# Kernel tuning notes

Measured on AMD Instinct MI355X. Metric: run time of the kernel, lower is better.

The kernel has to match this reference:

```python
import jax, jax.numpy as jnp
import numpy as np

K = 256      # embedding size k
STATE = 128  # latent state size
IN = 64      # external input size
OBS = 64     # observation size
L = 512      # sequence length (time-major)
B = 256      # batch size


def _glorot(key, shape):
    return jax.random.normal(key, shape, dtype=jnp.float32) / float(np.sqrt(shape[0]))


def setup_inputs():
    key = jax.random.key(0)
    ks = jax.random.split(key, 12)
    p = {}
    p["external_input_seq"] = jax.random.normal(ks[0], (L, B, IN), dtype=jnp.float32)
    p["observations_seq"] = jax.random.normal(ks[1], (L, B, OBS), dtype=jnp.float32)
    p["eps"] = jax.random.normal(ks[2], (L, B, STATE), dtype=jnp.float32)  # reparam noise
    # PreProcess: Linear + tanh
    p["Wu"] = _glorot(ks[3], (IN, K)); p["bu"] = jnp.zeros((K,), jnp.float32)
    p["Wx"] = _glorot(ks[4], (OBS, K)); p["bx"] = jnp.zeros((K,), jnp.float32)
    # input_rnn: vanilla tanh RNN, 1 layer, k -> k
    p["W_ih"] = _glorot(ks[5], (K, K)); p["b_ih"] = jnp.zeros((K,), jnp.float32)
    p["W_hh"] = _glorot(ks[6], (K, K)); p["b_hh"] = jnp.zeros((K,), jnp.float32)
    # posterior_a_layer: MLP(2k, k, k, 1) = Linear -> tanh -> Linear
    p["Wa1"] = _glorot(ks[7], (2 * K, K)); p["ba1"] = jnp.zeros((K,), jnp.float32)
    p["Wa2"] = _glorot(ks[8], (K, K)); p["ba2"] = jnp.zeros((K,), jnp.float32)

    def dblock_params(k1, in_dim, hid, out):
        kk = jax.random.split(k1, 4)
        return (_glorot(kk[0], (in_dim, hid)), jnp.zeros((hid,), jnp.float32),
                _glorot(kk[1], (in_dim, hid)), jnp.zeros((hid,), jnp.float32),
                _glorot(kk[2], (hid, out)), jnp.zeros((out,), jnp.float32),
                _glorot(kk[3], (hid, out)), jnp.zeros((out,), jnp.float32))

    names = ["f1_W", "f1_b", "f2_W", "f2_b", "mu_W", "mu_b", "ls_W", "ls_b"]
    for pref, kk in (("post_", ks[9]), ("prior_", ks[10])):
        vals = dblock_params(kk, STATE + K, 2 * K, STATE)
        for n, v in zip(names, vals):
            p[pref + n] = v
    return p


def _dblock(x, f1_W, f1_b, f2_W, f2_b, mu_W, mu_b, ls_W, ls_b):
    # TD-VAE DBlock: gated hidden, then mu / logsigma heads
    t = jnp.tanh(x @ f1_W + f1_b) * jax.nn.sigmoid(x @ f2_W + f2_b)
    return t @ mu_W + mu_b, t @ ls_W + ls_b


def reference(external_input_seq, observations_seq, eps, Wu, bu, Wx, bx,
              W_ih, b_ih, W_hh, b_hh, Wa1, ba1, Wa2, ba2,
              post_f1_W, post_f1_b, post_f2_W, post_f2_b, post_mu_W, post_mu_b, post_ls_W, post_ls_b,
              prior_f1_W, prior_f1_b, prior_f2_W, prior_f2_b, prior_mu_W, prior_mu_b, prior_ls_W, prior_ls_b):
    batch = external_input_seq.shape[1]
    u_emb = jnp.tanh(external_input_seq @ Wu + bu)   # [L,B,K]
    x_emb = jnp.tanh(observations_seq @ Wx + bx)     # [L,B,K]

    # input_rnn (tanh RNN) over time, d0 = 0 (memory_state=None)
    def rnn_step(d, x):
        d_new = jnp.tanh(x @ W_ih + b_ih + d @ W_hh + b_hh)
        return d_new, d_new
    d0 = jnp.zeros((batch, W_hh.shape[0]), dtype=u_emb.dtype)
    dn, d_seq = jax.lax.scan(rnn_step, d0, u_emb)    # dn [B,K], d_seq [L,B,K]

    # posterior_a_layer: pointwise MLP; flip(0) then flip(0) is a no-op for a pointwise map
    ad = jnp.concatenate([d_seq, x_emb], axis=-1)    # [L,B,2K]
    a_seq = jnp.tanh(ad @ Wa1 + ba1) @ Wa2 + ba2     # [L,B,K]

    state_size = post_mu_W.shape[1]
    z0 = jnp.zeros((batch, state_size), dtype=u_emb.dtype)

    def step(z_prev, inp):
        a_t, d_t, e_t = inp
        mean_res, logsigma = _dblock(jnp.concatenate([z_prev, a_t], axis=-1),
                                     post_f1_W, post_f1_b, post_f2_W, post_f2_b,
                                     post_mu_W, post_mu_b, post_ls_W, post_ls_b)
        prior_mean = _dblock(jnp.concatenate([z_prev, d_t], axis=-1),
                             prior_f1_W, prior_f1_b, prior_f2_W, prior_f2_b,
                             prior_mu_W, prior_mu_b, prior_ls_W, prior_ls_b)[0]
        mu = prior_mean + mean_res
        # cov = diag(exp(logsigma)) -> std = exp(0.5*logsigma); reparameterized sample
        z_new = mu + jnp.exp(0.5 * logsigma) * e_t
        return z_new, (mu, logsigma)

    zn, (state_mu, state_logsigma) = jax.lax.scan(step, z0, (a_seq, d_seq, eps))
    return state_mu, state_logsigma, dn, zn
```

## Files before the change

kernel.cpp:

```cpp
#include <hip/hip_runtime.h>

#define LSEQ 512
#define BATCH 256
#define KDIM 256
#define STATE 128

using f32x4  = __attribute__((ext_vector_type(4))) float;
using short8 = __attribute__((ext_vector_type(8))) short;
using u32x2  = __attribute__((ext_vector_type(2))) unsigned int;
using u32x4  = __attribute__((ext_vector_type(4))) unsigned int;

__device__ __forceinline__ float bf2f(unsigned short u){
  return __uint_as_float(((unsigned int)u) << 16);
}
__device__ __forceinline__ unsigned short f2bf(float f){
  unsigned int u = __float_as_uint(f);
  u += 0x7FFFu + ((u >> 16) & 1u);
  return (unsigned short)(u >> 16);
}
__device__ __forceinline__ float fast_tanh(float x){
  float ax = fabsf(x);
  float e  = __expf(2.0f * ax);
  float t  = 1.0f - 2.0f / (e + 1.0f);
  return copysignf(t, x);
}
__device__ __forceinline__ float fast_sig(float x){
  return 1.0f / (1.0f + __expf(-x));
}
__device__ __forceinline__ f32x4 mfma16(short8 a, short8 b, f32x4 c){
  return __builtin_amdgcn_mfma_f32_16x16x32_bf16(a, b, c, 0, 0, 0);
}

__device__ __forceinline__ int swz128 (int b){ return b ^ ((((b >> 7) & 7) << 4)); }
__device__ __forceinline__ int swz256 (int b){ return b ^ ((((b >> 8) & 7) << 4)); }
__device__ __forceinline__ int swz512 (int b){ return b ^ ((((b >> 9) & 7) << 4)); }

__device__ __forceinline__ void st_b128_ic(void* p, u32x4 v){
  asm volatile("global_store_dwordx4 %0, %1, off sc0 sc1" :: "v"(p), "v"(v) : "memory");
}
__device__ __forceinline__ void st_b64_ic(void* p, u32x2 v){
  asm volatile("global_store_dwordx2 %0, %1, off sc0 sc1" :: "v"(p), "v"(v) : "memory");
}
#define LD2_IC(dst, p) asm volatile("global_load_dwordx2 %0, %1, off sc0 sc1" : "=v"(dst) : "v"(p) : "memory")

__device__ __forceinline__ f32x4 cvt4(u32x2 q){
  f32x4 r;
  r[0] = __uint_as_float(q[0] << 16);
  r[1] = __uint_as_float(q[0] & 0xFFFF0000u);
  r[2] = __uint_as_float(q[1] << 16);
  r[3] = __uint_as_float(q[1] & 0xFFFF0000u);
  return r;
}

struct WDesc { const float* src; unsigned short* dst; int K, N, ld, rowoff, coloff; };
struct WDescs { WDesc d[24]; };

__global__ __launch_bounds__(256,4) void convert_weights(WDescs ds){
  WDesc w = ds.d[blockIdx.y];
  int total = w.K * w.N;
  int idx = blockIdx.x * 256 + threadIdx.x;
  if (idx < total){
    int n = idx / w.K;
    int k = idx - n * w.K;
    w.dst[idx] = f2bf(w.src[(size_t)(w.rowoff + k) * w.ld + w.coloff + n]);
  }
}

__global__ __launch_bounds__(256,1) void init_flags(int* flags){
  flags[blockIdx.x * 256 + threadIdx.x] = 0;
}

__global__ __launch_bounds__(256,4) void compose_GA(
    const float* __restrict__ Wa2, const float* __restrict__ ba2,
    const unsigned short* __restrict__ fAp,
    const float* __restrict__ pf1b, const float* __restrict__ pf2b,
    unsigned short* __restrict__ GA, float* __restrict__ gb)
{
  const int n = blockIdx.x;
  const int k2 = threadIdx.x;
  const unsigned short* fr = fAp + (size_t)n * 256;
  const float* wr = Wa2 + (size_t)k2 * 256;
  float s = 0.f;
  for (int j = 0; j < 256; j++) s += wr[j] * bf2f(fr[j]);
  GA[(size_t)n * 256 + k2] = f2bf(s);
  if (k2 == 0){
    float b = 0.f;
    for (int j = 0; j < 256; j++) b += ba2[j] * bf2f(fr[j]);
    gb[n] = b + ((n < 512) ? pf1b[n] : pf2b[n - 512]);
  }
}

struct GArg {
  const void* A; const unsigned short* Bt; const float* bias; const float* bias2;
  unsigned short* C; int lda, ldc, coff, K, act, a_f32;
};
struct GArg2 {
  const unsigned short* A; const unsigned short* Bt; const float* bias; const float* bias2;
  unsigned short* C; int lda, ldc, coff, K, act;
};

__device__ void gemm_multi_body(const GArg ga, int bx, int by, int tid, char* lsraw){
  char* lsA = lsraw;
  char* lsB = lsraw + 16384;
  const int wave = tid >> 6, lane = tid & 63;
  const int col_l = lane & 15, rgrp = lane >> 4;
  const int m0 = bx * 128, n0 = by * 128;
  const int wm = (wave >> 1) * 64, wn = (wave & 1) * 64;

  f32x4 acc[4][4];
  const f32x4 z4 = {0.f,0.f,0.f,0.f};
  #pragma unroll
  for (int i=0;i<4;i++){ acc[i][0]=z4; acc[i][1]=z4; acc[i][2]=z4; acc[i][3]=z4; }

  const int srow = tid >> 1;
  const int sbe  = (tid & 1) * 32;

  for (int k0 = 0; k0 < ga.K; k0 += 64){
    uint4 av[4], bv[4];
    if (ga.a_f32){
      const float* Ap = (const float*)ga.A + (size_t)(m0 + srow) * ga.lda + k0 + sbe;
      uint4 fv[8];
      #pragma unroll
      for (int i=0;i<8;i++) fv[i] = *(const uint4*)((const char*)Ap + i*16);
      #pragma unroll
      for (int i=0;i<4;i++){
        const float* f = (const float*)&fv[i*2];
        uint4 o;
        o.x = (unsigned)f2bf(f[0]) | ((unsigned)f2bf(f[1]) << 16);
        o.y = (unsigned)f2bf(f[2]) | ((unsigned)f2bf(f[3]) << 16);
        o.z = (unsigned)f2bf(f[4]) | ((unsigned)f2bf(f[5]) << 16);
        o.w = (unsigned)f2bf(f[6]) | ((unsigned)f2bf(f[7]) << 16);
        av[i] = o;
      }
    } else {
      const unsigned short* Ap = (const unsigned short*)ga.A + (size_t)(m0 + srow) * ga.lda + k0 + sbe;
      #pragma unroll
      for (int i=0;i<4;i++) av[i] = *(const uint4*)((const char*)Ap + i*16);
    }
    const unsigned short* Bp = ga.Bt + (size_t)(n0 + srow) * ga.K + k0 + sbe;
    #pragma unroll
    for (int i=0;i<4;i++) bv[i] = *(const uint4*)((const char*)Bp + i*16);

    __syncthreads();
    #pragma unroll
    for (int i=0;i<4;i++){
      *(uint4*)(lsA + swz128(srow*128 + sbe*2 + i*16)) = av[i];
      *(uint4*)(lsB + swz128(srow*128 + sbe*2 + i*16)) = bv[i];
    }
    __syncthreads();
    #pragma unroll
    for (int kk=0; kk<2; kk++){
      short8 af[4], bfr[4];
      #pragma unroll
      for (int mt=0; mt<4; mt++)
        af[mt] = *(const short8*)(lsA + swz128((wm + mt*16 + col_l)*128 + kk*64 + rgrp*16));
      #pragma unroll
      for (int nt=0; nt<4; nt++)
        bfr[nt] = *(const short8*)(lsB + swz128((wn + nt*16 + col_l)*128 + kk*64 + rgrp*16));
      #pragma unroll
      for (int mt=0; mt<4; mt++)
        #pragma unroll
        for (int nt=0; nt<4; nt++)
          acc[mt][nt] = mfma16(af[mt], bfr[nt], acc[mt][nt]);
    }
  }
  #pragma unroll
  for (int nt=0; nt<4; nt++){
    int col = n0 + wn + nt*16 + col_l;
    const float* bsrc = (col < 512) ? ga.bias : ga.bias2;
    float bb = bsrc ? bsrc[col & 511] : 0.0f;
    #pragma unroll
    for (int mt=0; mt<4; mt++){
      #pragma unroll
      for (int r=0; r<4; r++){
        int row = m0 + wm + mt*16 + rgrp*4 + r;
        float v = acc[mt][nt][r] + bb;
        if (ga.act == 1) v = fast_tanh(v);
        ga.C[(size_t)row * ga.ldc + ga.coff + col] = f2bf(v);
      }
    }
  }
}

__device__ void gemm_glds_body(const GArg2 ga, int bx, int by, int tid, char* lsraw){
  const int wave = tid >> 6, lane = tid & 63;
  const int col_l = lane & 15, rgrp = lane >> 4;
  const int m0 = bx * 128, n0 = by * 128;
  const int wm = (wave >> 1) * 64, wn = (wave & 1) * 64;

  const int lrow = lane >> 3;
  const int scol = (((lane & 7) ^ lrow) << 3);

  auto STAGE = [&](int k0, int buf){
    #pragma unroll
    for (int c = 0; c < 4; c++){
      int srow = wave*32 + c*8 + lrow;
      const unsigned short* pa = ga.A  + (size_t)(m0 + srow) * ga.lda + k0 + scol;
      const unsigned short* pb = ga.Bt + (size_t)(n0 + srow) * ga.K  + k0 + scol;
      __builtin_amdgcn_global_load_lds(
          (const __attribute__((address_space(1))) unsigned int*)pa,
          (__attribute__((address_space(3))) unsigned int*)(lsraw + buf*32768 + wave*4096 + c*1024),
          16, 0, 0);
      __builtin_amdgcn_global_load_lds(
          (const __attribute__((address_space(1))) unsigned int*)pb,
          (__attribute__((address_space(3))) unsigned int*)(lsraw + buf*32768 + 16384 + wave*4096 + c*1024),
          16, 0, 0);
    }
  };

  f32x4 acc[4][4];
  const f32x4 z4 = {0.f,0.f,0.f,0.f};
  #pragma unroll
  for (int i=0;i<4;i++){ acc[i][0]=z4; acc[i][1]=z4; acc[i][2]=z4; acc[i][3]=z4; }

  const int niter = ga.K >> 6;
  STAGE(0, 0);

  for (int i = 0; i < niter; i++){
    if (i + 1 < niter){
      STAGE((i+1)*64, (i+1) & 1);
      asm volatile("s_waitcnt vmcnt(8)" ::: "memory");
    } else {
      asm volatile("s_waitcnt vmcnt(0)" ::: "memory");
    }
    __syncthreads();
    const char* la = lsraw + (i&1)*32768;
    const char* lb = la + 16384;
    #pragma unroll
    for (int kk=0; kk<2; kk++){
      short8 af[4], bfr[4];
      #pragma unroll
      for (int mt=0; mt<4; mt++)
        af[mt] = *(const short8*)(la + swz128((wm + mt*16 + col_l)*128 + kk*64 + rgrp*16));
      #pragma unroll
      for (int nt=0; nt<4; nt++)
        bfr[nt] = *(const short8*)(lb + swz128((wn + nt*16 + col_l)*128 + kk*64 + rgrp*16));
      #pragma unroll
      for (int mt=0; mt<4; mt++)
        #pragma unroll
        for (int nt=0; nt<4; nt++)
          acc[mt][nt] = mfma16(af[mt], bfr[nt], acc[mt][nt]);
    }
    __syncthreads();
  }

  unsigned short* lt = (unsigned short*)lsraw;
  #pragma unroll
  for (int nt=0; nt<4; nt++){
    int cl = wn + nt*16 + col_l;
    int col = n0 + cl;
    const float* bsrc = (col < 512) ? ga.bias : ga.bias2;
    float bb = bsrc ? bsrc[col & 511] : 0.0f;
    #pragma unroll
    for (int mt=0; mt<4; mt++){
      #pragma unroll
      for (int r=0; r<4; r++){
        int rl = wm + mt*16 + rgrp*4 + r;
        float v = acc[mt][nt][r] + bb;
        if (ga.act == 1) v = fast_tanh(v);
        lt[rl*128 + cl] = f2bf(v);
      }
    }
  }
  __syncthreads();
  #pragma unroll
  for (int i=0; i<8; i++){
    int idx = i*256 + tid;
    int row = idx >> 4, ch = idx & 15;
    u32x4 v = *(const u32x4*)(lt + row*128 + ch*8);
    *(u32x4*)(ga.C + (size_t)(m0 + row) * ga.ldc + ga.coff + n0 + ch*8) = v;
  }
}

__device__ void rnn_body(
    const unsigned short* rnn_in, const unsigned short* Whh_t, const float* b_hh,
    unsigned short* cat_d, float* dn_out, unsigned short* d_state,
    int t0, int nsteps, int bx, int tid, char* lsraw)
{
  char* dls = lsraw;
  const int wave = tid >> 6, lane = tid & 63;
  const int col_l = lane & 15, rgrp = lane >> 4;
  const int brow0 = bx * 16;
  const int ncol = wave * 64;

  short8 bfr[4][8];
  #pragma unroll
  for (int nt=0; nt<4; nt++){
    const unsigned short* bp = Whh_t + (size_t)(ncol + nt*16 + col_l) * 256;
    #pragma unroll
    for (int kk=0; kk<8; kk++)
      bfr[nt][kk] = *(const short8*)(bp + kk*32 + rgrp*8);
  }
  float bias[4];
  #pragma unroll
  for (int nt=0; nt<4; nt++) bias[nt] = b_hh[ncol + nt*16 + col_l];

  if (t0 == 0){
    for (int i = tid; i < 16*256; i += 256){
      int row = i >> 8, col = i & 255;
      *(unsigned short*)(dls + swz512(row*512 + col*2)) = 0;
    }
  } else {
    const unsigned short* ds = d_state + (size_t)brow0 * 256;
    for (int i = tid; i < 16*256; i += 256){
      int row = i >> 8, col = i & 255;
      *(unsigned short*)(dls + swz512(row*512 + col*2)) = ds[row*256 + col];
    }
  }
  __syncthreads();

  for (int tl=0; tl<nsteps; tl++){
    unsigned short rv[4][4];
    const unsigned short* rp = rnn_in + (size_t)(tl*BATCH + brow0) * 256;
    #pragma unroll
    for (int nt=0; nt<4; nt++)
      #pragma unroll
      for (int r=0; r<4; r++)
        rv[nt][r] = rp[(size_t)(rgrp*4 + r)*256 + ncol + nt*16 + col_l];

    f32x4 acc[4];
    const f32x4 z4 = {0.f,0.f,0.f,0.f};
    acc[0]=z4; acc[1]=z4; acc[2]=z4; acc[3]=z4;
    #pragma unroll
    for (int kk=0; kk<8; kk++){
      short8 af = *(const short8*)(dls + swz512((lane & 15)*512 + kk*64 + rgrp*16));
      #pragma unroll
      for (int nt=0; nt<4; nt++)
        acc[nt] = mfma16(af, bfr[nt][kk], acc[nt]);
    }
    __syncthreads();
    #pragma unroll
    for (int nt=0; nt<4; nt++){
      #pragma unroll
      for (int r=0; r<4; r++){
        float h = acc[nt][r] + bf2f(rv[nt][r]) + bias[nt];
        float d = fast_tanh(h);
        int row = rgrp*4 + r, col = ncol + nt*16 + col_l;
        unsigned short db = f2bf(d);
        *(unsigned short*)(dls + swz512(row*512 + col*2)) = db;
        cat_d[(size_t)(tl*BATCH + brow0 + row)*512 + col] = db;
        if (t0 + tl == LSEQ-1) dn_out[(size_t)(brow0 + row)*256 + col] = d;
      }
    }
    __syncthreads();
  }
  unsigned short* dso = d_state + (size_t)brow0 * 256;
  for (int i = tid; i < 16*256; i += 256){
    int row = i >> 8, col = i & 255;
    dso[row*256 + col] = *(const unsigned short*)(dls + swz512(row*512 + col*2));
  }
}

__device__ void zrec_body(
    const unsigned short* preP, const unsigned short* preQ,
    const unsigned short* Wzz, const unsigned short* W2,
    const float* pmub, const float* plsb, const float* qmub,
    const float* eps, float* out_mu, float* out_ls, float* out_zn,
    unsigned short* z_state, unsigned short* mb, int* flags,
    int t0, int nsteps, int poff, int bid, int tid, char* lsraw)
{
  unsigned short* zls = (unsigned short*)lsraw;
  unsigned short* tls = (unsigned short*)(lsraw + 4096);
  unsigned short* bls = (unsigned short*)(lsraw + 12288);
  const int wave = tid >> 6, lane = tid & 63;
  const int col_l = lane & 15, rgrp = lane >> 4;
  const int c   = (bid >> 3) & 3;
  const int g   = (bid & 7) + ((bid >> 5) << 3);
  const int brow0 = g * 16;
  const int NT2 = (c < 2) ? 2 : 1;

  const unsigned short* pre = (c < 2) ? preP : preQ;
  const int cb = (c & 1) * 256;

  short8 w1[2][2][4];
  {
    const unsigned short* wz = Wzz + (size_t)c * 65536;
    #pragma unroll
    for (int m=0; m<2; m++)
      #pragma unroll
      for (int nt=0; nt<2; nt++){
        int n = wave*32 + nt*16 + col_l;
        #pragma unroll
        for (int kk=0; kk<4; kk++)
          w1[m][nt][kk] = *(const short8*)(wz + (size_t)(m*256 + n)*128 + kk*32 + rgrp*8);
      }
  }
  short8 w2r[2][8];
  {
    const unsigned short* wp = W2 + (size_t)c * 65536;
    #pragma unroll
    for (int nt=0; nt<2; nt++){
      if (nt < NT2){
        int ccol = wave*(16*((c<2)?2:1)) + nt*16;
        int mat = (c < 2) ? (ccol >> 7) : 0;
        int n   = (ccol & 127) + col_l;
        #pragma unroll
        for (int kk=0; kk<8; kk++)
          w2r[nt][kk] = *(const short8*)(wp + (size_t)(mat*128 + n)*256 + kk*32 + rgrp*8);
      }
    }
  }
  int* const fline  = flags + g*32;
  int* const myflag = fline + c;

  if (t0 == 0){
    for (int i = tid; i < 16*128; i += 512){
      int row = i >> 7, col = i & 127;
      *(unsigned short*)((char*)zls + swz256(row*256 + col*2)) = 0;
    }
  } else {
    const unsigned short* zs = z_state + (size_t)brow0 * 128;
    for (int i = tid; i < 16*128; i += 512){
      int row = i >> 7, col = i & 127;
      *(unsigned short*)((char*)zls + swz256(row*256 + col*2)) = zs[row*128 + col];
    }
  }
  __syncthreads();

  auto LD_PRE = [&](int tl, unsigned short (&pa_)[2][4], unsigned short (&pb_)[2][4]){
    const unsigned short* bA = pre + ((size_t)(poff + tl)*BATCH + brow0)*1024 + cb;
    #pragma unroll
    for (int nt=0; nt<2; nt++)
      #pragma unroll
      for (int r=0; r<4; r++){
        int row = rgrp*4 + r, col = wave*32 + nt*16 + col_l;
        pa_[nt][r] = bA[(size_t)row*1024 + col];
        pb_[nt][r] = bA[(size_t)row*1024 + 512 + col];
      }
  };

  const int rrow = tid >> 5;
  const int rc0  = (tid & 31) * 4;
  const f32x4 bp4 = *(const f32x4*)(pmub + rc0);
  const f32x4 bl4 = *(const f32x4*)(plsb + rc0);
  const f32x4 bq4 = *(const f32x4*)(qmub + rc0);

  unsigned short pa0[2][4], pb0[2][4], pa1[2][4], pb1[2][4];
  LD_PRE(0, pa0, pb0);

  const f32x4 z4 = {0.f,0.f,0.f,0.f};
  for (int tl=0; tl<nsteps; ++tl){
    size_t growr = (size_t)(t0+tl)*BATCH + brow0 + rrow;
    f32x4 er = *(const f32x4*)(eps + growr*STATE + rc0);
    int nx = (tl+1 < nsteps) ? tl+1 : tl;
    LD_PRE(nx, pa1, pb1);
    const int par = (t0 + tl) & 1;

    short8 af1[4];
    #pragma unroll
    for (int kk=0; kk<4; kk++)
      af1[kk] = *(const short8*)((const char*)zls + swz256((lane & 15)*256 + kk*64 + rgrp*16));
    f32x4 a1[2][2];
    a1[0][0]=z4; a1[0][1]=z4; a1[1][0]=z4; a1[1][1]=z4;
    #pragma unroll
    for (int kk=0; kk<4; kk++)
      #pragma unroll
      for (int m=0; m<2; m++)
        #pragma unroll
        for (int nt=0; nt<2; nt++)
          a1[m][nt] = mfma16(af1[kk], w1[m][nt][kk], a1[m][nt]);

    #pragma unroll
    for (int nt=0; nt<2; nt++)
      #pragma unroll
      for (int r=0; r<4; r++){
        float h1 = a1[0][nt][r] + bf2f(pa0[nt][r]);
        float h2 = a1[1][nt][r] + bf2f(pb0[nt][r]);
        float tv = fast_tanh(h1) * fast_sig(h2);
        int row = rgrp*4 + r, tcol = wave*32 + nt*16 + col_l;
        *(unsigned short*)((char*)tls + swz512(row*512 + tcol*2)) = f2bf(tv);
      }
    __syncthreads();

    f32x4 a2[2];
    a2[0]=z4; a2[1]=z4;
    #pragma unroll
    for (int kk=0; kk<8; kk++){
      short8 af2 = *(const short8*)((const char*)tls + swz512((lane & 15)*512 + kk*64 + rgrp*16));
      #pragma unroll
      for (int nt=0; nt<2; nt++)
        if (nt < NT2) a2[nt] = mfma16(af2, w2r[nt][kk], a2[nt]);
    }
    if (c < 2){
      #pragma unroll
      for (int nt=0; nt<2; nt++)
        #pragma unroll
        for (int r=0; r<4; r++)
          bls[(rgrp*4 + r)*256 + wave*32 + nt*16 + col_l] = f2bf(a2[nt][r]);
    } else {
      #pragma unroll
      for (int r=0; r<4; r++)
        bls[(rgrp*4 + r)*128 + wave*16 + col_l] = f2bf(a2[0][r]);
    }
    __syncthreads();

    unsigned short* slot = mb + (size_t)((g*2 + par)*4 + c)*4096;
    if (c < 2){
      u32x4 v = *(const u32x4*)((const char*)bls + tid*16);
      st_b128_ic(slot + tid*8, v);
    } else {
      u32x2 v = *(const u32x2*)((const char*)bls + tid*8);
      st_b64_ic(slot + tid*4, v);
    }
    asm volatile("s_waitcnt vmcnt(0)" ::: "memory");
    __syncthreads();
    const int target = t0 + tl + 1;
    if (tid == 0)
      __hip_atomic_store(myflag, target, __ATOMIC_RELAXED, __HIP_MEMORY_SCOPE_AGENT);

    if (lane == 0){
      u32x4 F;
      for (;;){
        asm volatile("global_load_dwordx4 %0, %1, off sc0 sc1\n\ts_waitcnt vmcnt(0)"
                     : "=v"(F) : "v"(fline) : "memory");
        int ok = 1;
        #pragma unroll
        for (int p=0; p<4; p++)
          if (p != c && (int)F[p] < target) ok = 0;
        if (ok) break;
        __builtin_amdgcn_s_sleep(1);
      }
    }

    const unsigned short* mbb = mb + (size_t)((g*2 + par)*4)*4096;
    const unsigned short* s0 = mbb;
    const unsigned short* s1 = mbb + 4096;
    const unsigned short* s2 = mbb + 8192;
    const unsigned short* s3 = mbb + 12288;
    u32x2 q0,q1,q2,q3,q4,q5;
    LD2_IC(q0, s0 + rrow*256 + rc0);
    LD2_IC(q1, s1 + rrow*256 + rc0);
    LD2_IC(q2, s0 + rrow*256 + 128 + rc0);
    LD2_IC(q3, s1 + rrow*256 + 128 + rc0);
    LD2_IC(q4, s2 + rrow*128 + rc0);
    LD2_IC(q5, s3 + rrow*128 + rc0);
    asm volatile("s_waitcnt vmcnt(0)" ::: "memory");
    __builtin_amdgcn_sched_barrier(0);

    f32x4 mup = cvt4(q0) + cvt4(q1);
    f32x4 lsv = cvt4(q2) + cvt4(q3) + bl4;
    f32x4 muq = cvt4(q4) + cvt4(q5);
    f32x4 muv = (muq + bq4) + (mup + bp4);
    f32x4 zv;
    #pragma unroll
    for (int i=0; i<4; i++) zv[i] = muv[i] + __expf(0.5f * lsv[i]) * er[i];

    unsigned int lo = (unsigned)f2bf(zv[0]) | ((unsigned)f2bf(zv[1]) << 16);
    unsigned int hi = (unsigned)f2bf(zv[2]) | ((unsigned)f2bf(zv[3]) << 16);
    uint2 zp; zp.x = lo; zp.y = hi;
    *(uint2*)((char*)zls + swz256(rrow*256 + rc0*2)) = zp;
    if (c == 0){
      *(f32x4*)(out_mu + growr*STATE + rc0) = muv;
      *(f32x4*)(out_ls + growr*STATE + rc0) = lsv;
      if (t0 + tl == LSEQ-1)
        *(f32x4*)(out_zn + ((size_t)(brow0 + rrow))*STATE + rc0) = zv;
    }
    __syncthreads();

    #pragma unroll
    for (int nt=0; nt<2; nt++)
      #pragma unroll
      for (int r=0; r<4; r++){ pa0[nt][r] = pa1[nt][r]; pb0[nt][r] = pb1[nt][r]; }
  }

  if (c == 0){
    unsigned short* zso = z_state + (size_t)brow0 * 128;
    for (int i = tid; i < 16*128; i += 512){
      int row = i >> 7, col = i & 127;
      zso[row*128 + col] = *(const unsigned short*)((const char*)zls + swz256(row*256 + col*2));
    }
  }
}

struct MegaArgs {
  const unsigned short *zP, *zQ, *Wzz, *W2;
  const float *pmub, *plsb, *qmub, *eps;
  float *out_mu, *out_ls, *out_zn;
  unsigned short *zst, *mb; int *flags;
  int t0z, nsz, poff;
  int stage, gx;
  GArg  e0, e1;
  GArg2 p0, p1;
  const unsigned short *rnn_in, *Whh; const float* b_hh;
  unsigned short* cat_d; float* dn_out; unsigned short* dstt; int t0r, nsr;
};

__global__ __launch_bounds__(512,1) void mega(MegaArgs A){
  __shared__ __align__(16) char smem[131072];
  const int tid = threadIdx.x;
  if ((int)blockIdx.x < 64){
    if (A.nsz > 0)
      zrec_body(A.zP, A.zQ, A.Wzz, A.W2, A.pmub, A.plsb, A.qmub, A.eps,
                A.out_mu, A.out_ls, A.out_zn, A.zst, A.mb, A.flags,
                A.t0z, A.nsz, A.poff, (int)blockIdx.x, tid, smem);
    return;
  }
  const int pb = (int)blockIdx.x - 64;
  const int half = tid >> 8, ltid = tid & 255;
  char* ls = smem + half*65536;
  const int lg = pb*2 + half;
  if (A.stage == 0){
    int bxx = lg % A.gx, t = lg / A.gx;
    gemm_multi_body((t >= 2) ? A.e1 : A.e0, bxx, t & 1, ltid, ls);
  } else if (A.stage == 1 || A.stage == 3){
    int bxx = lg % A.gx, by = lg / A.gx;
    gemm_glds_body(A.p0, bxx, by, ltid, ls);
  } else if (A.stage == 2){
    rnn_body(A.rnn_in, A.Whh, A.b_hh, A.cat_d, A.dn_out, A.dstt, A.t0r, A.nsr, lg, ltid, ls);
  } else if (A.stage == 4){
    int bxx = lg % A.gx, t = lg / A.gx;
    gemm_glds_body((t >> 3) ? A.p1 : A.p0, bxx, t & 7, ltid, ls);
  }
}

extern "C" void kernel_launch(void* const* d_in, const int* in_sizes, int n_in,
                              void* d_out, int out_size, void* d_ws, size_t ws_size,
                              hipStream_t stream)
{
  const float* ext = (const float*)d_in[0];
  const float* obs = (const float*)d_in[1];
  const float* eps = (const float*)d_in[2];
  const float* Wu  = (const float*)d_in[3];
  const float* bu  = (const float*)d_in[4];
  const float* Wx  = (const float*)d_in[5];
  const float* bx  = (const float*)d_in[6];
  const float* W_ih= (const float*)d_in[7];
  const float* b_ih= (const float*)d_in[8];
  const float* W_hh= (const float*)d_in[9];
  const float* b_hh= (const float*)d_in[10];
  const float* Wa1 = (const float*)d_in[11];
  const float* ba1 = (const float*)d_in[12];
  const float* Wa2 = (const float*)d_in[13];
  const float* ba2 = (const float*)d_in[14];
  const float* pf1W= (const float*)d_in[15]; const float* pf1b = (const float*)d_in[16];
  const float* pf2W= (const float*)d_in[17]; const float* pf2b = (const float*)d_in[18];
  const float* pmuW= (const float*)d_in[19]; const float* pmub = (const float*)d_in[20];
  const float* plsW= (const float*)d_in[21]; const float* plsb = (const float*)d_in[22];
  const float* qf1W= (const float*)d_in[23]; const float* qf1b = (const float*)d_in[24];
  const float* qf2W= (const float*)d_in[25]; const float* qf2b = (const float*)d_in[26];
  const float* qmuW= (const float*)d_in[27]; const float* qmub = (const float*)d_in[28];

  int NC = 0;
  const int cands[5] = {4,8,16,32,64};
  size_t rows = 0;
  for (int ci=0; ci<5; ci++){
    size_t r = (size_t)(LSEQ/cands[ci])*BATCH;
    size_t elems = 2600000 + r*5120;
    if (elems * 2 <= ws_size){ NC = cands[ci]; rows = r; break; }
  }
  if (!NC) return;
  const int nsteps = LSEQ/NC;
  const int gx = (int)(rows/128);

  unsigned short* ws = (unsigned short*)d_ws;
  size_t off = 0;
  auto alloc = [&](size_t elems){
    unsigned short* p = ws + off;
    off += (elems + 127) & ~(size_t)127;
    return p;
  };

  unsigned short* Wu_t  = alloc(64*256);
  unsigned short* Wx_t  = alloc(64*256);
  unsigned short* Wih_t = alloc(256*256);
  unsigned short* Whh_t = alloc(256*256);
  unsigned short* Wa1_t = alloc(512*256);
  unsigned short* fAp   = alloc(1024*256);
  unsigned short* fAq   = alloc(1024*256);
  unsigned short* GAp   = alloc(1024*256);
  float*          gbp   = (float*)alloc(2048);
  unsigned short* Wzz   = alloc(4*2*256*128);
  unsigned short* W2z   = alloc(4*2*128*256);
  unsigned short* d_state = alloc(256*256);
  unsigned short* z_state = alloc(256*128);
  unsigned short* mbx  = alloc(16*2*4*4096);
  int*   flg  = (int*)alloc(4096);
  unsigned short* bufA  = alloc(rows*256);
  unsigned short* bufB  = alloc(rows*256);
  unsigned short* bufC  = alloc(rows*512);
  unsigned short* preP0 = alloc(rows*1024);
  unsigned short* preP1 = alloc(rows*1024);
  unsigned short* preQ0 = alloc(rows*1024);
  unsigned short* preQ1 = alloc(rows*1024);
  if (off * sizeof(unsigned short) > ws_size) return;

  float* out_mu = (float*)d_out;
  float* out_ls = out_mu + (size_t)LSEQ*BATCH*STATE;
  float* out_dn = out_ls + (size_t)LSEQ*BATCH*STATE;
  float* out_zn = out_dn + (size_t)BATCH*KDIM;

  WDescs wd;
  int wi = 0;
  auto add = [&](const float* s, unsigned short* d, int Kk, int Nn, int ld, int ro, int co){
    wd.d[wi].src = s; wd.d[wi].dst = d; wd.d[wi].K = Kk; wd.d[wi].N = Nn;
    wd.d[wi].ld = ld; wd.d[wi].rowoff = ro; wd.d[wi].coloff = co; wi++;
  };
  add(Wu,   Wu_t,  64, 256, 256, 0, 0);
  add(Wx,   Wx_t,  64, 256, 256, 0, 0);
  add(W_ih, Wih_t, 256, 256, 256, 0, 0);
  add(W_hh, Whh_t, 256, 256, 256, 0, 0);
  add(Wa1,  Wa1_t, 512, 256, 256, 0, 0);
  add(pf1W, fAp,            256, 512, 512, 128, 0);
  add(pf2W, fAp + 512*256,  256, 512, 512, 128, 0);
  add(qf1W, fAq,            256, 512, 512, 128, 0);
  add(qf2W, fAq + 512*256,  256, 512, 512, 128, 0);
  for (int c=0; c<4; c++){
    const float* s1 = (c < 2) ? pf1W : qf1W;
    const float* s2 = (c < 2) ? pf2W : qf2W;
    add(s1, Wzz + (size_t)(c*2+0)*32768, 128, 256, 512, 0, (c&1)*256);
    add(s2, Wzz + (size_t)(c*2+1)*32768, 128, 256, 512, 0, (c&1)*256);
  }
  add(pmuW, W2z + (size_t)(0*2+0)*32768, 256, 128, 128, 0,   0);
  add(plsW, W2z + (size_t)(0*2+1)*32768, 256, 128, 128, 0,   0);
  add(pmuW, W2z + (size_t)(1*2+0)*32768, 256, 128, 128, 256, 0);
  add(plsW, W2z + (size_t)(1*2+1)*32768, 256, 128, 128, 256, 0);
  add(qmuW, W2z + (size_t)(2*2+0)*32768, 256, 128, 128, 0,   0);
  add(qmuW, W2z + (size_t)(3*2+0)*32768, 256, 128, 128, 256, 0);

  convert_weights<<<dim3(512, wi), 256, 0, stream>>>(wd);
  compose_GA<<<1024, 256, 0, stream>>>(Wa2, ba2, fAp, pf1b, pf2b, GAp, gbp);
  init_flags<<<8, 256, 0, stream>>>(flg);

  const int wseg[5] = {12, 12, 12, 26, 66};
  int segs[5]; int sacc = 0;
  for (int i=0; i<4; i++){
    int s = (nsteps * wseg[i] / 128) & ~1;
    if (s < 2) s = 2;
    segs[i] = s; sacc += s;
  }
  segs[4] = nsteps - sacc;

  auto zfill = [&](MegaArgs& A, int c_z){
    A.zP = (c_z & 1) ? preP1 : preP0;
    A.zQ = (c_z & 1) ? preQ1 : preQ0;
    A.Wzz = Wzz; A.W2 = W2z; A.pmub = pmub; A.plsb = plsb; A.qmub = qmub;
    A.eps = eps; A.out_mu = out_mu; A.out_ls = out_ls; A.out_zn = out_zn;
    A.zst = z_state; A.mb = mbx; A.flags = flg;
  };

  for (int c=0; c<NC; ++c){
    const size_t row0 = (size_t)c * nsteps * BATCH;
    unsigned short* pP = (c & 1) ? preP1 : preP0;
    unsigned short* pQ = (c & 1) ? preQ1 : preQ0;
    int zo = 0;
    for (int st=0; st<5; st++){
      MegaArgs A{};
      zfill(A, c-1);
      A.t0z = (c-1)*nsteps + zo;
      A.poff = zo;
      A.nsz = (c == 0) ? 0 : segs[st];
      zo += segs[st];
      A.stage = st; A.gx = gx;
      int nphys;
      if (st == 0){
        A.e0 = GArg{ext + row0*64, Wu_t, bu, bu, bufA, 64, 256, 0,   64, 1, 1};
        A.e1 = GArg{obs + row0*64, Wx_t, bx, bx, bufC, 64, 512, 256, 64, 1, 1};
        nphys = gx*2;
      } else if (st == 1){
        A.p0 = GArg2{bufA, Wih_t, b_ih, b_ih, bufB, 256, 256, 0, 256, 0};
        nphys = gx;
      } else if (st == 2){
        A.rnn_in = bufB; A.Whh = Whh_t; A.b_hh = b_hh; A.cat_d = bufC;
        A.dn_out = out_dn; A.dstt = d_state; A.t0r = c*nsteps; A.nsr = nsteps;
        nphys = 8;
      } else if (st == 3){
        A.p0 = GArg2{bufC, Wa1_t, ba1, ba1, bufA, 512, 256, 0, 512, 1};
        nphys = gx;
      } else {
        A.p0 = GArg2{bufA, GAp, gbp, gbp + 512, pP, 256, 1024, 0, 256, 0};
        A.p1 = GArg2{bufC, fAq, qf1b, qf2b, pQ, 512, 1024, 0, 256, 0};
        nphys = gx*8;
      }
      mega<<<64 + nphys, 512, 0, stream>>>(A);
    }
  }
  {
    MegaArgs A{};
    zfill(A, NC-1);
    A.t0z = (NC-1)*nsteps; A.poff = 0; A.nsz = nsteps;
    A.stage = 5; A.gx = gx;
    mega<<<64, 512, 0, stream>>>(A);
  }
}
```

Measured before the change: 3.552 ms.

## Split mega kernel into per-stage kernels and pre-convert inputs to bf16

Replaces the single stage-switched mega kernel with one specialized kernel per stage, so each variant compiles only its own GEMM or RNN body and may use fewer registers and less branching alongside the persistent z-recurrence blocks. The embedding GEMM now reads bf16 copies of the external input and observation sequences, produced once by a new conversion kernel, instead of converting fp32 to bf16 inside the GEMM with the old multi-body path. This adds two extra full passes over the input sequences and a larger workspace reservation.

```diff
diff --git a/kernel.cpp b/kernel.cpp
--- a/kernel.cpp
+++ b/kernel.cpp
@@ -64,6 +64,12 @@
     int k = idx - n * w.K;
     w.dst[idx] = f2bf(w.src[(size_t)(w.rowoff + k) * w.ld + w.coloff + n]);
   }
+}
+
+__global__ __launch_bounds__(256,4) void tobf16(const float* __restrict__ in,
+                                                unsigned short* __restrict__ out, int n){
+  for (int i = blockIdx.x * 256 + threadIdx.x; i < n; i += gridDim.x * 256)
+    out[i] = f2bf(in[i]);
 }
 
 __global__ __launch_bounds__(256,1) void init_flags(int* flags){
@@ -90,97 +96,10 @@
   }
 }
 
-struct GArg {
-  const void* A; const unsigned short* Bt; const float* bias; const float* bias2;
-  unsigned short* C; int lda, ldc, coff, K, act, a_f32;
-};
 struct GArg2 {
   const unsigned short* A; const unsigned short* Bt; const float* bias; const float* bias2;
   unsigned short* C; int lda, ldc, coff, K, act;
 };
-
-__device__ void gemm_multi_body(const GArg ga, int bx, int by, int tid, char* lsraw){
-  char* lsA = lsraw;
-  char* lsB = lsraw + 16384;
-  const int wave = tid >> 6, lane = tid & 63;
-  const int col_l = lane & 15, rgrp = lane >> 4;
-  const int m0 = bx * 128, n0 = by * 128;
-  const int wm = (wave >> 1) * 64, wn = (wave & 1) * 64;
-
-  f32x4 acc[4][4];
-  const f32x4 z4 = {0.f,0.f,0.f,0.f};
-  #pragma unroll
-  for (int i=0;i<4;i++){ acc[i][0]=z4; acc[i][1]=z4; acc[i][2]=z4; acc[i][3]=z4; }
-
-  const int srow = tid >> 1;
-  const int sbe  = (tid & 1) * 32;
-
-  for (int k0 = 0; k0 < ga.K; k0 += 64){
-    uint4 av[4], bv[4];
-    if (ga.a_f32){
-      const float* Ap = (const float*)ga.A + (size_t)(m0 + srow) * ga.lda + k0 + sbe;
-      uint4 fv[8];
-      #pragma unroll
-      for (int i=0;i<8;i++) fv[i] = *(const uint4*)((const char*)Ap + i*16);
-      #pragma unroll
-      for (int i=0;i<4;i++){
-        const float* f = (const float*)&fv[i*2];
-        uint4 o;
-        o.x = (unsigned)f2bf(f[0]) | ((unsigned)f2bf(f[1]) << 16);
-        o.y = (unsigned)f2bf(f[2]) | ((unsigned)f2bf(f[3]) << 16);
-        o.z = (unsigned)f2bf(f[4]) | ((unsigned)f2bf(f[5]) << 16);
-        o.w = (unsigned)f2bf(f[6]) | ((unsigned)f2bf(f[7]) << 16);
-        av[i] = o;
-      }
-    } else {
-      const unsigned short* Ap = (const unsigned short*)ga.A + (size_t)(m0 + srow) * ga.lda + k0 + sbe;
-      #pragma unroll
-      for (int i=0;i<4;i++) av[i] = *(const uint4*)((const char*)Ap + i*16);
-    }
-    const unsigned short* Bp = ga.Bt + (size_t)(n0 + srow) * ga.K + k0 + sbe;
-    #pragma unroll
-    for (int i=0;i<4;i++) bv[i] = *(const uint4*)((const char*)Bp + i*16);
-
-    __syncthreads();
-    #pragma unroll
-    for (int i=0;i<4;i++){
-      *(uint4*)(lsA + swz128(srow*128 + sbe*2 + i*16)) = av[i];
-      *(uint4*)(lsB + swz128(srow*128 + sbe*2 + i*16)) = bv[i];
-    }
-    __syncthreads();
-    #pragma unroll
-    for (int kk=0; kk<2; kk++){
-      short8 af[4], bfr[4];
-      #pragma unroll
-      for (int mt=0; mt<4; mt++)
-        af[mt] = *(const short8*)(lsA + swz128((wm + mt*16 + col_l)*128 + kk*64 + rgrp*16));
-      #pragma unroll
-      for (int nt=0; nt<4; nt++)
-        bfr[nt] = *(const short8*)(lsB + swz128((wn + nt*16 + col_l)*128 + kk*64 + rgrp*16));
-      #pragma unroll
-      for (int mt=0; mt<4; mt++)
-        #pragma unroll
-        for (int nt=0; nt<4; nt++)
-          acc[mt][nt] = mfma16(af[mt], bfr[nt], acc[mt][nt]);
-    }
-  }
-  #pragma unroll
-  for (int nt=0; nt<4; nt++){
-    int col = n0 + wn + nt*16 + col_l;
-    const float* bsrc = (col < 512) ? ga.bias : ga.bias2;
-    float bb = bsrc ? bsrc[col & 511] : 0.0f;
-    #pragma unroll
-    for (int mt=0; mt<4; mt++){
-      #pragma unroll
-      for (int r=0; r<4; r++){
-        int row = m0 + wm + mt*16 + rgrp*4 + r;
-        float v = acc[mt][nt][r] + bb;
-        if (ga.act == 1) v = fast_tanh(v);
-        ga.C[(size_t)row * ga.ldc + ga.coff + col] = f2bf(v);
-      }
-    }
-  }
-}
 
 __device__ void gemm_glds_body(const GArg2 ga, int bx, int by, int tid, char* lsraw){
   const int wave = tid >> 6, lane = tid & 63;
@@ -578,39 +497,59 @@
   float *out_mu, *out_ls, *out_zn;
   unsigned short *zst, *mb; int *flags;
   int t0z, nsz, poff;
-  int stage, gx;
-  GArg  e0, e1;
+  int gx;
   GArg2 p0, p1;
   const unsigned short *rnn_in, *Whh; const float* b_hh;
   unsigned short* cat_d; float* dn_out; unsigned short* dstt; int t0r, nsr;
 };
 
-__global__ __launch_bounds__(512,1) void mega(MegaArgs A){
+#define ZREC_PROLOG \
+  __shared__ __align__(16) char smem[131072]; \
+  const int tid = threadIdx.x; \
+  if ((int)blockIdx.x < 64){ \
+    if (A.nsz > 0) \
+      zrec_body(A.zP, A.zQ, A.Wzz, A.W2, A.pmub, A.plsb, A.qmub, A.eps, \
+                A.out_mu, A.out_ls, A.out_zn, A.zst, A.mb, A.flags, \
+                A.t0z, A.nsz, A.poff, (int)blockIdx.x, tid, smem); \
+    return; \
+  } \
+  const int pb = (int)blockIdx.x - 64; \
+  const int half = tid >> 8, ltid = tid & 255; \
+  char* ls = smem + half*65536; \
+  const int lg = pb*2 + half;
+
+__global__ __launch_bounds__(512,1) void mega_emb(MegaArgs A){
+  ZREC_PROLOG
+  int bxx = lg % A.gx, t = lg / A.gx;
+  GArg2 ga = (t >= 2) ? A.p1 : A.p0;
+  gemm_glds_body(ga, bxx, t & 1, ltid, ls);
+}
+__global__ __launch_bounds__(512,1) void mega_rn(MegaArgs A){
+  ZREC_PROLOG
+  int bxx = lg % A.gx, by = lg / A.gx;
+  gemm_glds_body(A.p0, bxx, by, ltid, ls);
+}
+__global__ __launch_bounds__(512,1) void mega_rnn(MegaArgs A){
+  ZREC_PROLOG
+  rnn_body(A.rnn_in, A.Whh, A.b_hh, A.cat_d, A.dn_out, A.dstt, A.t0r, A.nsr, lg, ltid, ls);
+}
+__global__ __launch_bounds__(512,1) void mega_a1(MegaArgs A){
+  ZREC_PROLOG
+  int bxx = lg % A.gx, by = lg / A.gx;
+  gemm_glds_body(A.p0, bxx, by, ltid, ls);
+}
+__global__ __launch_bounds__(512,1) void mega_pre(MegaArgs A){
+  ZREC_PROLOG
+  int bxx = lg % A.gx, t = lg / A.gx;
+  gemm_glds_body((t >> 3) ? A.p1 : A.p0, bxx, t & 7, ltid, ls);
+}
+__global__ __launch_bounds__(512,1) void mega_drain(MegaArgs A){
   __shared__ __align__(16) char smem[131072];
   const int tid = threadIdx.x;
-  if ((int)blockIdx.x < 64){
-    if (A.nsz > 0)
-      zrec_body(A.zP, A.zQ, A.Wzz, A.W2, A.pmub, A.plsb, A.qmub, A.eps,
-                A.out_mu, A.out_ls, A.out_zn, A.zst, A.mb, A.flags,
-                A.t0z, A.nsz, A.poff, (int)blockIdx.x, tid, smem);
-    return;
-  }
-  const int pb = (int)blockIdx.x - 64;
-  const int half = tid >> 8, ltid = tid & 255;
-  char* ls = smem + half*65536;
-  const int lg = pb*2 + half;
-  if (A.stage == 0){
-    int bxx = lg % A.gx, t = lg / A.gx;
-    gemm_multi_body((t >= 2) ? A.e1 : A.e0, bxx, t & 1, ltid, ls);
-  } else if (A.stage == 1 || A.stage == 3){
-    int bxx = lg % A.gx, by = lg / A.gx;
-    gemm_glds_body(A.p0, bxx, by, ltid, ls);
-  } else if (A.stage == 2){
-    rnn_body(A.rnn_in, A.Whh, A.b_hh, A.cat_d, A.dn_out, A.dstt, A.t0r, A.nsr, lg, ltid, ls);
-  } else if (A.stage == 4){
-    int bxx = lg % A.gx, t = lg / A.gx;
-    gemm_glds_body((t >> 3) ? A.p1 : A.p0, bxx, t & 7, ltid, ls);
-  }
+  if ((int)blockIdx.x < 64 && A.nsz > 0)
+    zrec_body(A.zP, A.zQ, A.Wzz, A.W2, A.pmub, A.plsb, A.qmub, A.eps,
+              A.out_mu, A.out_ls, A.out_zn, A.zst, A.mb, A.flags,
+              A.t0z, A.nsz, A.poff, (int)blockIdx.x, tid, smem);
 }
 
 extern "C" void kernel_launch(void* const* d_in, const int* in_sizes, int n_in,
@@ -645,7 +584,7 @@
   size_t rows = 0;
   for (int ci=0; ci<5; ci++){
     size_t r = (size_t)(LSEQ/cands[ci])*BATCH;
-    size_t elems = 2600000 + r*5120;
+    size_t elems = 20000000 + r*5120;
     if (elems * 2 <= ws_size){ NC = cands[ci]; rows = r; break; }
   }
   if (!NC) return;
@@ -675,6 +614,8 @@
   unsigned short* z_state = alloc(256*128);
   unsigned short* mbx  = alloc(16*2*4*4096);
   int*   flg  = (int*)alloc(4096);
+  unsigned short* ebf   = alloc((size_t)LSEQ*BATCH*64);
+  unsigned short* obf   = alloc((size_t)LSEQ*BATCH*64);
   unsigned short* bufA  = alloc(rows*256);
   unsigned short* bufB  = alloc(rows*256);
   unsigned short* bufC  = alloc(rows*512);
@@ -718,6 +659,8 @@
   add(qmuW, W2z + (size_t)(3*2+0)*32768, 256, 128, 128, 256, 0);
 
   convert_weights<<<dim3(512, wi), 256, 0, stream>>>(wd);
+  tobf16<<<2048, 256, 0, stream>>>(ext, ebf, LSEQ*BATCH*64);
+  tobf16<<<2048, 256, 0, stream>>>(obs, obf, LSEQ*BATCH*64);
   compose_GA<<<1024, 256, 0, stream>>>(Wa2, ba2, fAp, pf1b, pf2b, GAp, gbp);
   init_flags<<<8, 256, 0, stream>>>(flg);
 
@@ -750,35 +693,33 @@
       A.poff = zo;
       A.nsz = (c == 0) ? 0 : segs[st];
       zo += segs[st];
-      A.stage = st; A.gx = gx;
-      int nphys;
+      A.gx = gx;
       if (st == 0){
-        A.e0 = GArg{ext + row0*64, Wu_t, bu, bu, bufA, 64, 256, 0,   64, 1, 1};
-        A.e1 = GArg{obs + row0*64, Wx_t, bx, bx, bufC, 64, 512, 256, 64, 1, 1};
-        nphys = gx*2;
+        A.p0 = GArg2{ebf + row0*64, Wu_t, bu, bu, bufA, 64, 256, 0,   64, 1};
+        A.p1 = GArg2{obf + row0*64, Wx_t, bx, bx, bufC, 64, 512, 256, 64, 1};
+        mega_emb<<<64 + gx*2, 512, 0, stream>>>(A);
       } else if (st == 1){
         A.p0 = GArg2{bufA, Wih_t, b_ih, b_ih, bufB, 256, 256, 0, 256, 0};
-        nphys = gx;
+        mega_rn<<<64 + gx, 512, 0, stream>>>(A);
       } else if (st == 2){
         A.rnn_in = bufB; A.Whh = Whh_t; A.b_hh = b_hh; A.cat_d = bufC;
         A.dn_out = out_dn; A.dstt = d_state; A.t0r = c*nsteps; A.nsr = nsteps;
-        nphys = 8;
+        mega_rnn<<<64 + 8, 512, 0, stream>>>(A);
       } else if (st == 3){
         A.p0 = GArg2{bufC, Wa1_t, ba1, ba1, bufA, 512, 256, 0, 512, 1};
-        nphys = gx;
+        mega_a1<<<64 + gx, 512, 0, stream>>>(A);
       } else {
         A.p0 = GArg2{bufA, GAp, gbp, gbp + 512, pP, 256, 1024, 0, 256, 0};
         A.p1 = GArg2{bufC, fAq, qf1b, qf2b, pQ, 512, 1024, 0, 256, 0};
-        nphys = gx*8;
+        mega_pre<<<64 + gx*8, 512, 0, stream>>>(A);
       }
-      mega<<<64 + nphys, 512, 0, stream>>>(A);
     }
   }
   {
     MegaArgs A{};
     zfill(A, NC-1);
     A.t0z = (NC-1)*nsteps; A.poff = 0; A.nsz = nsteps;
-    A.stage = 5; A.gx = gx;
-    mega<<<64, 512, 0, stream>>>(A);
-  }
-}
+    A.gx = gx;
+    mega_drain<<<64, 512, 0, stream>>>(A);
+  }
+}
```

Result: slower. 4.514 ms (+27.1%).
